# Optimization experiments

Hardware: AMD Instinct MI355X
Metric: run time of the kernel (lower is better)

## Reference

```python
import jax, jax.numpy as jnp
import numpy as np

B, N, E, H = 16, 1024, 1024, 16  # batch must equal num_heads due to the 'hbkd' einsum in the original
D = E // H


def setup_inputs() -> dict:
    key = jax.random.key(0)
    ks = jax.random.split(key, 9)
    s = 0.02
    return {
        "x": jax.random.normal(ks[0], (B, N, E), dtype=jnp.float32),
        "Wq": jax.random.normal(ks[1], (E, E), dtype=jnp.float32) * s,
        "bq": jax.random.normal(ks[2], (E,), dtype=jnp.float32) * s,
        "Wk": jax.random.normal(ks[3], (E, E), dtype=jnp.float32) * s,
        "bk": jax.random.normal(ks[4], (E,), dtype=jnp.float32) * s,
        "Wv": jax.random.normal(ks[5], (E, E), dtype=jnp.float32) * s,
        "bv": jax.random.normal(ks[6], (E,), dtype=jnp.float32) * s,
        "Wp": jax.random.normal(ks[7], (E, E), dtype=jnp.float32) * s,
        "bp": jax.random.normal(ks[8], (E,), dtype=jnp.float32) * s,
    }


def _split_heads(t):  # [b, n, (h d)] -> [b, h, n, d]
    b, n, e = t.shape
    return t.reshape(b, n, H, D).transpose(0, 2, 1, 3)


def reference(x, Wq, bq, Wk, bk, Wv, bv, Wp, bp):
    q = _split_heads(x @ Wq.T + bq)  # [b, h, n, d]
    k = _split_heads(x @ Wk.T + bk)
    v = _split_heads(x @ Wv.T + bv)
    # Faithful to original: K is contracted with its batch/head axes SWAPPED ('hbkd').
    energy = jnp.einsum('bhqd,hbkd->bhqk', q, k)  # [b, h, n, n]
    # Faithful: softmax over the HEAD axis (dim=1), scale applied AFTER softmax.
    scale = E ** 0.5
    att = jax.nn.softmax(energy, axis=1) / scale
    # dropout rate is 0.0 -> identity
    o = jnp.einsum('bhal,bhlv->bhav', att, v)  # [b, h, n, d]
    o = o.transpose(0, 2, 1, 3).reshape(B, N, E)  # [b, n, (h d)]
    return o @ Wp.T + bp
```

## Files before the change

### kernel.cpp

```cpp
#include <hip/hip_runtime.h>
#include <hip/hip_bf16.h>

#define DEVI __device__ __forceinline__

typedef float f32x4 __attribute__((ext_vector_type(4)));
typedef short bf16x8 __attribute__((ext_vector_type(8)));
typedef unsigned short u16x4 __attribute__((ext_vector_type(4)));


DEVI unsigned short f2bf(float f) {
  union { float f; unsigned u; } v; v.f = f;
  unsigned r = v.u + 0x7fffu + ((v.u >> 16) & 1u);
  return (unsigned short)(r >> 16);
}

DEVI float fexp2(float x) {
#if __has_builtin(__builtin_amdgcn_exp2f)
  return __builtin_amdgcn_exp2f(x);
#else
  return exp2f(x);
#endif
}

DEVI float frcp(float x) {
#if __has_builtin(__builtin_amdgcn_rcpf)
  return __builtin_amdgcn_rcpf(x);
#else
  return 1.0f / x;
#endif
}

DEVI unsigned cvtpk(float a, float b) {
  unsigned r;
  asm("v_cvt_pk_bf16_f32 %0, %1, %2" : "=v"(r) : "v"(a), "v"(b));
  return r;
}

DEVI void gload_lds16(const unsigned short* g, unsigned short* l) {
  __builtin_amdgcn_global_load_lds(
      (const __attribute__((address_space(1))) void*)g,
      (__attribute__((address_space(3))) void*)l, 16, 0, 0);
}

DEVI void wg_barrier() {
  asm volatile("s_waitcnt lgkmcnt(0)" ::: "memory");
  __builtin_amdgcn_s_barrier();
  __builtin_amdgcn_sched_barrier(0);
}

__global__ void cvt_all(const float* __restrict__ x,
                        const float* __restrict__ Wq, const float* __restrict__ Wk,
                        const float* __restrict__ Wv, const float* __restrict__ Wp,
                        unsigned short* __restrict__ xbf, unsigned short* __restrict__ wbf) {
  int i = blockIdx.x * blockDim.x + threadIdx.x;
  const int st = gridDim.x * blockDim.x;
  for (; i < 5242880; i += st) {
    const float* s;
    unsigned short* d;
    int off;
    if (i < 4194304) {
      s = x; d = xbf; off = i;
    } else {
      const int j = i - 4194304;
      const int wsel = j >> 18;
      off = j & 262143;
      s = (wsel == 0) ? Wq : (wsel == 1) ? Wk : (wsel == 2) ? Wv : Wp;
      d = wbf + (wsel << 20);
    }
    const float4 v = reinterpret_cast<const float4*>(s)[off];
    u16x4 o;
    o[0] = f2bf(v.x); o[1] = f2bf(v.y); o[2] = f2bf(v.z); o[3] = f2bf(v.w);
    reinterpret_cast<u16x4*>(d)[off] = o;
  }
}

#define STA(BUF, C, K0) gload_lds16(&A[(size_t)(m0 + (C)*64 + srow) * 1024 + (K0) + scol], &lsA[BUF][(C)*4096 + tid*8])
#define STB(BUF, C, K0) gload_lds16(&Bw[(size_t)(n0 + (C)*64 + srow) * 1024 + (K0) + scol], &lsB[BUF][(C)*4096 + tid*8])

#define DSREAD_A(BUF, MF, KS) (*(const bf16x8*)&lsA[BUF][arow + (MF)*1024 + ((KS) ? sx1 : sx0)])
#define DSREAD_B(BUF, NF, KS) (*(const bf16x8*)&lsB[BUF][brow + (NF)*1024 + ((KS) ? sx1 : sx0)])

#define MFMA16(P, AF)                                                          \
    __builtin_amdgcn_s_setprio(1);                                             \
    _Pragma("unroll") for (int mfi = 0; mfi < 2; mfi++)                        \
      _Pragma("unroll") for (int nf = 0; nf < 4; nf++)                         \
        _Pragma("unroll") for (int ks = 0; ks < 2; ks++)                       \
          acc[2*(P)+mfi][nf] = __builtin_amdgcn_mfma_f32_16x16x32_bf16(        \
              AF[mfi][ks], bfr[nf][ks], acc[2*(P)+mfi][nf], 0, 0, 0);          \
    __builtin_amdgcn_s_setprio(0);

#define PHASE(BUF, P, LB, STG)                                                 \
  { __builtin_amdgcn_s_barrier();                                              \
    bf16x8 af[2][2];                                                           \
    _Pragma("unroll") for (int i = 0; i < 2; i++)                              \
      _Pragma("unroll") for (int k2 = 0; k2 < 2; k2++)                         \
        af[i][k2] = DSREAD_A(BUF, 2*(P)+i, k2);                                \
    if (LB) {                                                                  \
      _Pragma("unroll") for (int n2 = 0; n2 < 4; n2++)                         \
        _Pragma("unroll") for (int k2 = 0; k2 < 2; k2++)                       \
          bfr[n2][k2] = DSREAD_B(BUF, n2, k2);                                 \
    }                                                                          \
    STG;                                                                       \
    MFMA16(P, af) }

#define GSTEP(CB, NB, K1)                                                      \
    asm volatile("s_waitcnt vmcnt(2)" ::: "memory");                           \
    PHASE(CB, 0, 1, { STB(NB,0,K1); STB(NB,1,K1); })                           \
    PHASE(CB, 1, 0, { STB(NB,2,K1); STB(NB,3,K1); })                           \
    asm volatile("s_waitcnt vmcnt(4)" ::: "memory");                           \
    PHASE(CB, 2, 0, { STA(NB,0,K1); STA(NB,2,K1); })                           \
    PHASE(CB, 3, 0, { STA(NB,1,K1); STA(NB,3,K1); })

DEVI void gemm256_main(const unsigned short* __restrict__ A,
                       const unsigned short* __restrict__ Bw,
                       int m0, int n0,
                       unsigned short (&lsA)[2][16384],
                       unsigned short (&lsB)[2][16384],
                       f32x4 (&acc)[8][4]) {
  const int tid = threadIdx.x;
  const int l = tid & 63, lr = l & 15, lg = l >> 4;
  const int w = tid >> 6, wm = w >> 2, wn = w & 3;
  const int srow = tid >> 3;
  const int scol = (((tid & 7) ^ (srow & 7)) * 8);
  const int sx0 = (lg * 8) ^ ((lr & 7) << 3);
  const int sx1 = (32 + lg * 8) ^ ((lr & 7) << 3);
  const int arow = (wm * 128 + lr) * 64;
  const int brow = (wn * 64 + lr) * 64;

  STB(0,0,0); STB(0,1,0); STB(0,2,0); STB(0,3,0);
  STA(0,0,0); STA(0,1,0); STA(0,2,0); STA(0,3,0);
  asm volatile("s_waitcnt vmcnt(0)" ::: "memory");
  __builtin_amdgcn_s_barrier();

  bf16x8 bfr[4][2];

#pragma unroll 1
  for (int t7 = 0; t7 < 7; ++t7) {
    const int k1 = t7 * 128 + 64;
    GSTEP(0, 1, k1)
    GSTEP(1, 0, k1 + 64)
  }
  GSTEP(0, 1, 960)
  asm volatile("s_waitcnt vmcnt(2)" ::: "memory");
  PHASE(1, 0, 1, {})
  PHASE(1, 1, 0, {})
  asm volatile("s_waitcnt vmcnt(0)" ::: "memory");
  PHASE(1, 2, 0, {})
  PHASE(1, 3, 0, {})
}

__global__ __launch_bounds__(512, 2) void proj_qkv8(
    const unsigned short* __restrict__ A, const unsigned short* __restrict__ W3,
    const float* __restrict__ bq, const float* __restrict__ bk, const float* __restrict__ bv,
    unsigned short* __restrict__ outq, unsigned short* __restrict__ outk, unsigned short* __restrict__ outv) {
  __shared__ unsigned short lsA[2][16384];
  __shared__ unsigned short lsB[2][16384];
  const int f = blockIdx.x;
  const int flat = (f & 7) * 96 + (f >> 3);
  const int mt = flat / 12, sub = flat - mt * 12;
  const int z = sub >> 2, y = sub & 3;
  const int m0 = mt * 256, n0 = y * 256;
  const unsigned short* Bw = W3 + z * 1048576;
  f32x4 acc[8][4];
  const f32x4 z4 = {0.f, 0.f, 0.f, 0.f};
#pragma unroll
  for (int i = 0; i < 8; i++)
#pragma unroll
    for (int j = 0; j < 4; j++) acc[i][j] = z4;

  gemm256_main(A, Bw, m0, n0, lsA, lsB, acc);

  const int tid = threadIdx.x;
  const int l = tid & 63, lr = l & 15, lg = l >> 4;
  const int w = tid >> 6, wm = w >> 2, wn = w & 3;
  const float* bias = (z == 0) ? bq : ((z == 1) ? bk : bv);
  const float SC = 1.4426950408889634f;
#pragma unroll
  for (int mf = 0; mf < 8; mf++) {
    const int mb = m0 + wm * 128 + mf * 16 + lg * 4;
#pragma unroll
    for (int nf = 0; nf < 4; nf++) {
      const int ncol = n0 + wn * 64 + nf * 16 + lr;
      const float bsv = bias[ncol];
      const int h = ncol >> 6, d = ncol & 63;
      if (z == 0) {
        const int ks = d >> 5, lgq = (d >> 3) & 3, eq = d & 7;
#pragma unroll
        for (int r = 0; r < 4; r++) {
          const int m = mb + r;
          const int bb = m >> 10, nr = m & 1023;
          const int nt = nr >> 4, lrq = nr & 15;
          const int idx = (((bb * 64 + nt) * 32 + h * 2 + ks) * 64 + lgq * 16 + lrq) * 8 + eq;
          outq[idx] = f2bf((acc[mf][nf][r] + bsv) * SC);
        }
      } else if (z == 1) {
        const int ks = d >> 5, lhi = ((d >> 3) & 3) * 16, eq = d & 7;
#pragma unroll
        for (int r = 0; r < 4; r++) {
          const int m = mb + r;
          const int n = m & 1023, bx = m >> 10;
          const int lane = lhi + (n & 15);
          const int idx = ((((h * 64 + (n >> 4)) * 16 + bx) * 2 + ks) * 64 + lane) * 8 + eq;
          outk[idx] = f2bf(acc[mf][nf][r] + bsv);
        }
      } else {
        const int dt = d >> 4, lrv = d & 15;
        const int bb = mb >> 10, n = mb & 1023;
        const int kc = n >> 5, lgv = (n >> 3) & 3, ev = n & 7;
        u16x4 pk;
#pragma unroll
        for (int r = 0; r < 4; r++) pk[r] = f2bf(acc[mf][nf][r] + bsv);
        const int idx0 = ((((bb * 16 + h) * 32 + kc) * 4 + dt) * 64 + lgv * 16 + lrv) * 8 + ev;
        *(u16x4*)&outv[idx0] = pk;
      }
    }
  }
}

__global__ __launch_bounds__(512, 2) void proj_out8(
    const unsigned short* __restrict__ A, const unsigned short* __restrict__ Wp,
    const float* __restrict__ bias, float* __restrict__ out) {
  __shared__ unsigned short lsA[2][16384];
  __shared__ unsigned short lsB[2][16384];
  const int f = blockIdx.x;
  const int flat = (f & 7) * 32 + (f >> 3);
  const int mt = flat >> 2, y = flat & 3;
  const int m0 = mt * 256, n0 = y * 256;
  f32x4 acc[8][4];
  const f32x4 z4 = {0.f, 0.f, 0.f, 0.f};
#pragma unroll
  for (int i = 0; i < 8; i++)
#pragma unroll
    for (int j = 0; j < 4; j++) acc[i][j] = z4;

  gemm256_main(A, Wp, m0, n0, lsA, lsB, acc);

  const int tid = threadIdx.x;
  const int l = tid & 63, lr = l & 15, lg = l >> 4;
  const int w = tid >> 6, wm = w >> 2, wn = w & 3;
#pragma unroll
  for (int mf = 0; mf < 8; mf++) {
    const int mb = m0 + wm * 128 + mf * 16 + lg * 4;
#pragma unroll
    for (int nf = 0; nf < 4; nf++) {
      const int ncol = n0 + wn * 64 + nf * 16 + lr;
      const float bsv = bias[ncol];
#pragma unroll
      for (int r = 0; r < 4; r++) out[(size_t)(mb + r) * 1024 + ncol] = acc[mf][nf][r] + bsv;
    }
  }
}

#define ATTN_BODY(IT, KC, KN)                                                  \
  {                                                                            \
    int qo = 0;                                                                \
    asm volatile("" : "+v"(qo));                                               \
    f32x4 e[4][2];                                                             \
    _Pragma("unroll") for (int hl = 0; hl < 4; hl++) {                         \
      const int h = hq * 4 + hl;                                               \
      _Pragma("unroll") for (int qh = 0; qh < 2; qh++) {                       \
        bf16x8 q0 = *(const bf16x8*)((const char*)qlds + qo + (qh * 32 + h * 2 + 0) * 1024 + l * 16); \
        bf16x8 q1 = *(const bf16x8*)((const char*)qlds + qo + (qh * 32 + h * 2 + 1) * 1024 + l * 16); \
        f32x4 t = __builtin_amdgcn_mfma_f32_16x16x32_bf16(KC[hl * 2 + 0], q0, z4, 0, 0, 0); \
        t = __builtin_amdgcn_mfma_f32_16x16x32_bf16(KC[hl * 2 + 1], q1, t, 0, 0, 0); \
        t[0] = fexp2(t[0]); t[1] = fexp2(t[1]); t[2] = fexp2(t[2]); t[3] = fexp2(t[3]); \
        e[hl][qh] = t;                                                         \
      }                                                                        \
    }                                                                          \
    {                                                                          \
      const unsigned short* knp = kroot + (size_t)((((IT) + 1) & 15) * 4) * 16384; \
      _Pragma("unroll") for (int i = 0; i < 8; i++) KN[i] = *(const bf16x8*)(knp + i * 512); \
    }                                                                          \
    f32x4 s0 = (e[0][0] + e[1][0]) + (e[2][0] + e[3][0]);                      \
    f32x4 s1 = (e[0][1] + e[1][1]) + (e[2][1] + e[3][1]);                      \
    *(f32x4*)&sumbuf[((ksub * 4 + hq) * 2 + 0) * 256 + l * 4] = s0;            \
    *(f32x4*)&sumbuf[((ksub * 4 + hq) * 2 + 1) * 256 + l * 4] = s1;            \
    wg_barrier();                                                              \
    _Pragma("unroll") for (int p = 1; p < 4; p++) {                            \
      const int hqp = hq ^ p;                                                  \
      s0 += *(const f32x4*)&sumbuf[((ksub * 4 + hqp) * 2 + 0) * 256 + l * 4];  \
      s1 += *(const f32x4*)&sumbuf[((ksub * 4 + hqp) * 2 + 1) * 256 + l * 4];  \
    }                                                                          \
    f32x4 inv0, inv1;                                                          \
    inv0[0] = frcp(s0[0]) * 0.03125f; inv0[1] = frcp(s0[1]) * 0.03125f;        \
    inv0[2] = frcp(s0[2]) * 0.03125f; inv0[3] = frcp(s0[3]) * 0.03125f;        \
    inv1[0] = frcp(s1[0]) * 0.03125f; inv1[1] = frcp(s1[1]) * 0.03125f;        \
    inv1[2] = frcp(s1[2]) * 0.03125f; inv1[3] = frcp(s1[3]) * 0.03125f;        \
    _Pragma("unroll") for (int hl = 0; hl < 4; hl++) {                         \
      const int h = hq * 4 + hl;                                               \
      _Pragma("unroll") for (int qh = 0; qh < 2; qh++) {                       \
        f32x4 vv = e[hl][qh] * (qh ? inv1 : inv0);                             \
        uint2 pk;                                                              \
        pk.x = cvtpk(vv[0], vv[1]);                                            \
        pk.y = cvtpk(vv[2], vv[3]);                                            \
        *(uint2*)((char*)abuf + h * 4096 + (qh * 16 + lr) * 128 + ((kpart ^ wswz) << 1)) = pk; \
      }                                                                        \
    }                                                                          \
    {                                                                          \
      const unsigned short* vbp = vroot + (size_t)((IT) * 2) * 2048;           \
      _Pragma("unroll") for (int kst = 0; kst < 2; kst++)                      \
        _Pragma("unroll") for (int dt = 0; dt < 4; dt++)                       \
          vr[kst * 4 + dt] = *(const bf16x8*)(vbp + kst * 2048 + dt * 512);    \
    }                                                                          \
    wg_barrier();                                                              \
    bf16x8 pa[2][2];                                                           \
    _Pragma("unroll") for (int qt = 0; qt < 2; qt++)                           \
      _Pragma("unroll") for (int kst = 0; kst < 2; kst++)                      \
        pa[qt][kst] = *(const bf16x8*)((const char*)abuf + w * 4096 + qt * 2048 + lr * 128 + (((kst * 4 + lg) ^ (lr & 7)) << 4)); \
    _Pragma("unroll") for (int qt = 0; qt < 2; qt++)                           \
      _Pragma("unroll") for (int kst = 0; kst < 2; kst++)                      \
        _Pragma("unroll") for (int dt = 0; dt < 4; dt++)                       \
          oacc[qt][dt] = __builtin_amdgcn_mfma_f32_16x16x32_bf16(pa[qt][kst], vr[kst * 4 + dt], oacc[qt][dt], 0, 0, 0); \
  }

__global__ __launch_bounds__(1024, 4) void attn5(
    const unsigned short* __restrict__ Q2,
    const unsigned short* __restrict__ K2,
    const unsigned short* __restrict__ V2,
    unsigned short* __restrict__ O) {
  __shared__ unsigned short qlds[32768];
  __shared__ unsigned short abuf[32768];
  __shared__ float sumbuf[8192];

  const int tid = threadIdx.x;
  const int w = tid >> 6, l = tid & 63;
  const int lr = l & 15, lg = l >> 4;
  const int bid = blockIdx.x;
  const int swz = (bid & 7) * 64 + (bid >> 3);
  const int b = swz >> 5, qt32 = swz & 31;
  const int ksub = w & 3, hq = w >> 2;

  {
    const unsigned short* qsrc = Q2 + (size_t)(b * 64 + qt32 * 2) * 16384 + tid * 8;
    unsigned short* qdst = qlds + tid * 8;
#pragma unroll
    for (int r = 0; r < 4; r++) gload_lds16(qsrc + r * 8192, qdst + r * 8192);
  }

  const int kpart = ksub * 16 + lg * 4;
  const int wswz = (lr & 7) << 3;

  const f32x4 z4 = {0.f, 0.f, 0.f, 0.f};
  f32x4 oacc[2][4];
#pragma unroll
  for (int qt = 0; qt < 2; qt++)
#pragma unroll
    for (int dt = 0; dt < 4; dt++) oacc[qt][dt] = z4;

  const unsigned short* kroot = K2 + (size_t)(b * 64 + ksub) * 16384 + hq * 4096 + l * 8;
  const unsigned short* vroot = V2 + (size_t)((b * 16 + w) * 32) * 2048 + l * 8;

  bf16x8 kA[8], kB[8], vr[8];
#pragma unroll
  for (int i = 0; i < 8; i++) kA[i] = *(const bf16x8*)(kroot + i * 512);

  asm volatile("s_waitcnt vmcnt(0) lgkmcnt(0)" ::: "memory");
  __builtin_amdgcn_s_barrier();
  __builtin_amdgcn_sched_barrier(0);

#pragma unroll 1
  for (int it2 = 0; it2 < 8; it2++) {
    ATTN_BODY(it2 * 2, kA, kB)
    ATTN_BODY(it2 * 2 + 1, kB, kA)
  }

#pragma unroll
  for (int qt = 0; qt < 2; qt++)
#pragma unroll
    for (int dt = 0; dt < 4; dt++)
#pragma unroll
      for (int r = 0; r < 4; r++) {
        const int n = qt32 * 32 + qt * 16 + lg * 4 + r;
        O[(size_t)(b * 1024 + n) * 1024 + w * 64 + dt * 16 + lr] = f2bf(oacc[qt][dt][r]);
      }
}

extern "C" void kernel_launch(void* const* d_in, const int* in_sizes, int n_in,
                              void* d_out, int out_size, void* d_ws, size_t ws_size,
                              hipStream_t stream) {
  const float* x  = (const float*)d_in[0];
  const float* Wq = (const float*)d_in[1];
  const float* bq = (const float*)d_in[2];
  const float* Wk = (const float*)d_in[3];
  const float* bk = (const float*)d_in[4];
  const float* Wv = (const float*)d_in[5];
  const float* bv = (const float*)d_in[6];
  const float* Wp = (const float*)d_in[7];
  const float* bp = (const float*)d_in[8];

  char* ws = (char*)d_ws;
  unsigned short* xbf  = (unsigned short*)(ws);
  unsigned short* qbf  = (unsigned short*)(ws + 33554432);
  unsigned short* kbf  = (unsigned short*)(ws + 67108864);
  unsigned short* vtbf = (unsigned short*)(ws + 100663296);
  unsigned short* wbf  = (unsigned short*)(ws + 134217728);

  cvt_all<<<5120, 256, 0, stream>>>(x, Wq, Wk, Wv, Wp, xbf, wbf);

  proj_qkv8<<<768, 512, 0, stream>>>(xbf, wbf, bq, bk, bv, qbf, kbf, vtbf);
  attn5<<<512, 1024, 0, stream>>>(qbf, kbf, vtbf, xbf);
  proj_out8<<<256, 512, 0, stream>>>(xbf, wbf + 3145728, bp, (float*)d_out);
}
```

Before: 323.6 us.

## Use K=32 tiles in QKV projection GEMM to halve LDS and raise occupancy

Adds a new 256x256 GEMM main loop for the QKV projection that stages K-slices of 32 instead of 64. This halves the shared-memory double buffers, and the launch bounds ask for 4 blocks per CU instead of 2. The goal is higher occupancy so other waves can hide load latency. In exchange there are twice as many loop iterations and barriers per tile, and the register budget per thread is tighter, which could cause spills with 32 accumulator vectors.

Measured after the change: 1.109 ms. 3.43x slower.

```diff
diff --git a/kernel.cpp b/kernel.cpp
--- a/kernel.cpp
+++ b/kernel.cpp
@@ -149,12 +149,82 @@
   PHASE(1, 3, 0, {})
 }
 
-__global__ __launch_bounds__(512, 2) void proj_qkv8(
+#define STA32(BUF, C, K0) gload_lds16(&A[(size_t)(m0 + (C)*64 + srow8 + sext) * 1024 + (K0) + scol32], &lsA[BUF][(C)*4096 + tid*8])
+#define STB32(BUF, C, K0) gload_lds16(&Bw[(size_t)(n0 + (C)*64 + srow8 + sext) * 1024 + (K0) + scol32], &lsB[BUF][(C)*4096 + tid*8])
+
+#define PH32(BUF, P, LB, STG)                                                  \
+  { bf16x8 af_[2];                                                             \
+    af_[0] = *(const bf16x8*)&lsA[BUF][(2*(P)) * 1024 + lr * 64 + sxA];        \
+    af_[1] = *(const bf16x8*)&lsA[BUF][(2*(P)+1) * 1024 + lr * 64 + sxA];      \
+    if (LB) {                                                                  \
+      _Pragma("unroll") for (int n2 = 0; n2 < 4; n2++)                         \
+        bfr32[n2] = *(const bf16x8*)&lsB[BUF][brow32 + n2 * 1024 + sxB];       \
+    }                                                                          \
+    STG;                                                                       \
+    __builtin_amdgcn_s_setprio(1);                                             \
+    _Pragma("unroll") for (int mfi = 0; mfi < 2; mfi++)                        \
+      _Pragma("unroll") for (int nf = 0; nf < 4; nf++)                         \
+        acc[2*(P)+mfi][nf] = __builtin_amdgcn_mfma_f32_16x16x32_bf16(          \
+            af_[mfi], bfr32[nf], acc[2*(P)+mfi][nf], 0, 0, 0);                 \
+    __builtin_amdgcn_s_setprio(0);                                             \
+  }
+
+#define GST32(CB, NB, K1)                                                      \
+    asm volatile("s_waitcnt vmcnt(1)" ::: "memory");                           \
+    __builtin_amdgcn_s_barrier();                                              \
+    PH32(CB, 0, 1, { STB32(NB,0,K1); STB32(NB,1,K1); })                        \
+    PH32(CB, 1, 0, { STA32(NB,0,K1); })                                        \
+    asm volatile("s_waitcnt vmcnt(3)" ::: "memory");                           \
+    __builtin_amdgcn_s_barrier();                                              \
+    PH32(CB, 2, 0, { STA32(NB,1,K1); })                                        \
+    PH32(CB, 3, 0, {})
+
+DEVI void gemm256k32_main(const unsigned short* __restrict__ A,
+                          const unsigned short* __restrict__ Bw,
+                          int m0, int n0,
+                          unsigned short (&lsA)[2][8192],
+                          unsigned short (&lsB)[2][8192],
+                          f32x4 (&acc)[8][4]) {
+  const int tid = threadIdx.x;
+  const int l = tid & 63, lr = l & 15, lg = l >> 4;
+  const int w = tid >> 6, wm = w >> 2, wn = w & 3;
+  const int srow8 = tid >> 3;
+  const int g = (tid & 7) ^ (srow8 & 7);
+  const int sext = (g >= 4) ? 128 : 0;
+  const int scol32 = (g & 3) * 8;
+  const int sxA = (wm * 32 + lg * 8) ^ ((lr & 7) << 3);
+  const int sxB = ((wn >> 1) * 32 + lg * 8) ^ ((lr & 7) << 3);
+  const int brow32 = ((wn & 1) * 64 + lr) * 64;
+
+  STB32(0,0,0); STB32(0,1,0); STA32(0,0,0); STA32(0,1,0);
+  asm volatile("s_waitcnt vmcnt(0)" ::: "memory");
+  __builtin_amdgcn_s_barrier();
+
+  bf16x8 bfr32[4];
+
+#pragma unroll 1
+  for (int t15 = 0; t15 < 15; ++t15) {
+    const int k1 = t15 * 64 + 32;
+    GST32(0, 1, k1)
+    GST32(1, 0, k1 + 32)
+  }
+  GST32(0, 1, 992)
+  asm volatile("s_waitcnt vmcnt(1)" ::: "memory");
+  __builtin_amdgcn_s_barrier();
+  PH32(1, 0, 1, {})
+  PH32(1, 1, 0, {})
+  asm volatile("s_waitcnt vmcnt(0)" ::: "memory");
+  __builtin_amdgcn_s_barrier();
+  PH32(1, 2, 0, {})
+  PH32(1, 3, 0, {})
+}
+
+__global__ __launch_bounds__(512, 4) void proj_qkv8(
     const unsigned short* __restrict__ A, const unsigned short* __restrict__ W3,
     const float* __restrict__ bq, const float* __restrict__ bk, const float* __restrict__ bv,
     unsigned short* __restrict__ outq, unsigned short* __restrict__ outk, unsigned short* __restrict__ outv) {
-  __shared__ unsigned short lsA[2][16384];
-  __shared__ unsigned short lsB[2][16384];
+  __shared__ unsigned short lsA[2][8192];
+  __shared__ unsigned short lsB[2][8192];
   const int f = blockIdx.x;
   const int flat = (f & 7) * 96 + (f >> 3);
   const int mt = flat / 12, sub = flat - mt * 12;
@@ -168,7 +238,7 @@
 #pragma unroll
     for (int j = 0; j < 4; j++) acc[i][j] = z4;
 
-  gemm256_main(A, Bw, m0, n0, lsA, lsB, acc);
+  gemm256k32_main(A, Bw, m0, n0, lsA, lsB, acc);
 
   const int tid = threadIdx.x;
   const int l = tid & 63, lr = l & 15, lg = l >> 4;
```
